# Performance work log

Measured on AMD Instinct MI355X. Metric: run time of the kernel, lower is better.

The kernel has to match this reference:

```python
import jax, jax.numpy as jnp
import numpy as np

N_NODES = 100000
N_EDGES = 1600000
D_IN = 128
D_OUT = 128


def setup_inputs() -> dict:
    key = jax.random.key(0)
    k1, k2, k3, k4, k5, k6 = jax.random.split(key, 6)
    x = jax.random.normal(k1, (N_NODES, D_IN), dtype=jnp.float32)
    edge_index = jax.random.randint(k2, (2, N_EDGES), 0, N_NODES, dtype=jnp.int64)
    edge_weight = jax.random.uniform(k3, (N_EDGES,), dtype=jnp.float32)
    # Linear(in_features=128, out_features=128, bias=True) parameters
    bound = 1.0 / np.sqrt(D_IN)
    W = jax.random.uniform(k4, (D_OUT, D_IN), minval=-bound, maxval=bound, dtype=jnp.float32)
    b = jax.random.uniform(k5, (D_OUT,), minval=-bound, maxval=bound, dtype=jnp.float32)
    return {
        "x": x,
        "edge_index": edge_index,
        "edge_weight": edge_weight,
        "W": W,
        "b": b,
        "vertex_cnt": N_NODES,
        "rule_cnt": 0,
    }


def reference(x, edge_index, edge_weight, W, b, vertex_cnt, rule_cnt):
    # KPropagate: edge-based message passing.
    # messages[e] = edge_weight[e] * x[src[e]]; out[dst] = sum of messages into dst.
    src = edge_index[0]
    dst = edge_index[1]
    msgs = x[src] * edge_weight[:, None]          # [E, D_IN]
    agg = jax.ops.segment_sum(msgs, dst, num_segments=vertex_cnt)  # [N, D_IN]
    # Dense linear projection: y = agg @ W^T + b
    return agg @ W.T + b
```

## Files before the change

kernel.cpp:

```cpp
#include <hip/hip_runtime.h>
#include <hip/hip_bf16.h>

#define D 128
#define RT 64
#define BK 64
#define CAP 2048
#define PAD 16

typedef __attribute__((ext_vector_type(8))) short short8;
typedef __attribute__((ext_vector_type(4))) float floatx4;

__device__ __forceinline__ ushort f2bf(float v) {
  return __hip_bfloat16_raw(__float2bfloat16(v)).x;
}
__device__ __forceinline__ float bf2f(ushort u) {
  return __uint_as_float((unsigned)u << 16);
}

__global__ __launch_bounds__(256) void k1_gemm_fill(
    const float* __restrict__ x, const float* __restrict__ W,
    ushort* __restrict__ y, const int* __restrict__ ei,
    const float* __restrict__ ew, int* __restrict__ cursor,
    int2* __restrict__ bucket, int N, int E, int GB) {
  if (blockIdx.x >= GB) {
    int e = (blockIdx.x - GB) * 256 + threadIdx.x;
    if (e < E) {
      int s = ei[e];
      int d = ei[E + e];
      float w = ew[e];
      int bk = d >> 6;
      int p = atomicAdd(&cursor[bk * PAD], 1);
      if (p < CAP)
        bucket[(long long)bk * CAP + p] =
            make_int2(s | ((d & 63) << 26), __float_as_int(w));
    }
    return;
  }
  __shared__ __align__(16) ushort sX[RT * 136];
  __shared__ __align__(16) ushort sW[128 * 136];

  int tid = threadIdx.x;
  int rowBase = blockIdx.x * RT;

#pragma unroll
  for (int it = 0; it < 16; it++) {
    int i = tid + it * 256;
    int r = i >> 5;
    int c4 = i & 31;
    float4 v = *(const float4*)(W + r * 128 + c4 * 4);
    *(ushort4*)&sW[r * 136 + c4 * 4] =
        make_ushort4(f2bf(v.x), f2bf(v.y), f2bf(v.z), f2bf(v.w));
  }
#pragma unroll
  for (int it = 0; it < 8; it++) {
    int i = tid + it * 256;
    int r = i >> 5;
    int c4 = i & 31;
    int row = rowBase + r;
    float4 v = (row < N) ? *(const float4*)(x + (long long)row * 128 + c4 * 4)
                         : make_float4(0.f, 0.f, 0.f, 0.f);
    *(ushort4*)&sX[r * 136 + c4 * 4] =
        make_ushort4(f2bf(v.x), f2bf(v.y), f2bf(v.z), f2bf(v.w));
  }
  __syncthreads();

  int wv = tid >> 6;
  int lane = tid & 63;
  int m = lane & 15;
  int q = lane >> 4;

  const ushort* aRow = &sX[(wv * 16 + m) * 136 + q * 8];
  const ushort* bRow = &sW[m * 136 + q * 8];

  floatx4 acc[8];
#pragma unroll
  for (int ct = 0; ct < 8; ct++) acc[ct] = (floatx4){0.f, 0.f, 0.f, 0.f};

#pragma unroll
  for (int ks = 0; ks < 4; ks++) {
    short8 a = *(const short8*)(aRow + ks * 32);
#pragma unroll
    for (int ct = 0; ct < 8; ct++) {
      short8 b = *(const short8*)(bRow + ct * 16 * 136 + ks * 32);
      acc[ct] = __builtin_amdgcn_mfma_f32_16x16x32_bf16(a, b, acc[ct], 0, 0, 0);
    }
  }

  int row0 = rowBase + wv * 16 + q * 4;
#pragma unroll
  for (int r = 0; r < 4; r++) {
    int row = row0 + r;
    if (row < N) {
      ushort* yp = y + (long long)row * 128 + m;
#pragma unroll
      for (int ct = 0; ct < 8; ct++) yp[ct * 16] = f2bf(acc[ct][r]);
    }
  }
}

__global__ __launch_bounds__(256) void sort_gather(
    const ushort* __restrict__ y, const int2* __restrict__ bucket,
    const int* __restrict__ cursor, const float* __restrict__ bias,
    float* __restrict__ out, int N) {
  __shared__ __align__(16) int2 smd[CAP];
  __shared__ int sdeg[BK];
  __shared__ int soffs[BK];
  __shared__ int scur[BK];

  int tid = threadIdx.x;
  int bk = blockIdx.x;
  long long base = (long long)bk * CAP;
  int cnt = min(cursor[bk * PAD], CAP);

  if (tid < BK) sdeg[tid] = 0;
  __syncthreads();
  for (int i = tid; i < cnt; i += 256) {
    unsigned v = (unsigned)bucket[base + i].x;
    atomicAdd(&sdeg[v >> 26], 1);
  }
  __syncthreads();
  if (tid < BK) {
    int s = 0;
    for (int j = 0; j < tid; j++) s += sdeg[j];
    soffs[tid] = s;
    scur[tid] = s;
  }
  __syncthreads();
  for (int i = tid; i < cnt; i += 256) {
    int2 md = bucket[base + i];
    int d = (unsigned)md.x >> 26;
    int pos = atomicAdd(&scur[d], 1);
    smd[pos] = md;
  }
  __syncthreads();

  int wv = tid >> 6;
  int lane = tid & 63;
  const ushort2* yv = (const ushort2*)y;
  float2 bb = ((const float2*)bias)[lane];

  for (int nd = wv; nd < BK; nd += 4) {
    int node = bk * BK + nd;
    if (node >= N) continue;
    int st = soffs[nd];
    int c = sdeg[nd];
    float ax = 0.f, ay = 0.f;
    int j = 0;
    for (; j + 4 <= c; j += 4) {
      int2 m0 = smd[st + j];
      int2 m1 = smd[st + j + 1];
      int2 m2 = smd[st + j + 2];
      int2 m3 = smd[st + j + 3];
      int s0 = m0.x & 0x03FFFFFF, s1 = m1.x & 0x03FFFFFF;
      int s2 = m2.x & 0x03FFFFFF, s3 = m3.x & 0x03FFFFFF;
      float w0 = __int_as_float(m0.y), w1 = __int_as_float(m1.y);
      float w2 = __int_as_float(m2.y), w3 = __int_as_float(m3.y);
      ushort2 u0 = yv[(long long)s0 * 64 + lane];
      ushort2 u1 = yv[(long long)s1 * 64 + lane];
      ushort2 u2 = yv[(long long)s2 * 64 + lane];
      ushort2 u3 = yv[(long long)s3 * 64 + lane];
      ax += w0 * bf2f(u0.x) + w1 * bf2f(u1.x) + w2 * bf2f(u2.x) +
            w3 * bf2f(u3.x);
      ay += w0 * bf2f(u0.y) + w1 * bf2f(u1.y) + w2 * bf2f(u2.y) +
            w3 * bf2f(u3.y);
    }
    for (; j < c; j++) {
      int2 m0 = smd[st + j];
      int s0 = m0.x & 0x03FFFFFF;
      float w0 = __int_as_float(m0.y);
      ushort2 u0 = yv[(long long)s0 * 64 + lane];
      ax += w0 * bf2f(u0.x);
      ay += w0 * bf2f(u0.y);
    }
    float2 o = {ax + bb.x, ay + bb.y};
    ((float2*)out)[(long long)node * 64 + lane] = o;
  }
}

extern "C" void kernel_launch(void* const* d_in, const int* in_sizes, int n_in,
                              void* d_out, int out_size, void* d_ws,
                              size_t ws_size, hipStream_t stream) {
  const float* x = (const float*)d_in[0];
  const int* ei = (const int*)d_in[1];
  const float* ew = (const float*)d_in[2];
  const float* W = (const float*)d_in[3];
  const float* b = (const float*)d_in[4];

  int N = in_sizes[0] / D;
  int E = in_sizes[2];
  int NBK = (N + BK - 1) / BK;

  int* cursor = (int*)d_ws;
  int2* bucket = (int2*)(cursor + (size_t)NBK * PAD);
  ushort* y = (ushort*)(bucket + (size_t)NBK * CAP);

  hipMemsetAsync(cursor, 0, (size_t)NBK * PAD * sizeof(int), stream);

  int GB = (N + RT - 1) / RT;
  int FB = (E + 255) / 256;
  k1_gemm_fill<<<GB + FB, 256, 0, stream>>>(x, W, y, ei, ew, cursor, bucket, N,
                                            E, GB);
  sort_gather<<<NBK, 256, 0, stream>>>(y, bucket, cursor, b, (float*)d_out, N);
}
```

Before: 301.7 us.

## Split bucket atomic cursors per XCD to avoid cross-die atomic contention

Each destination bucket now gets eight sub-buckets, one per XCD, selected by reading the hardware XCC_ID register. Edge-fill atomics then hit a cursor that only one die touches, which is meant to cut contended cross-die atomics and cache-line bouncing. The gather kernel walks all eight sub-buckets when building its shared-memory sort. Each sub-bucket holds at most 256 entries, so an uneven spread of edges across XCDs could overflow one and silently drop edges, and the cursor array grows eightfold.

```diff
diff --git a/kernel.cpp b/kernel.cpp
--- a/kernel.cpp
+++ b/kernel.cpp
@@ -5,6 +5,7 @@
 #define RT 64
 #define BK 64
 #define CAP 2048
+#define SUBCAP 256
 #define PAD 16
 
 typedef __attribute__((ext_vector_type(8))) short short8;
@@ -15,6 +16,12 @@
 }
 __device__ __forceinline__ float bf2f(ushort u) {
   return __uint_as_float((unsigned)u << 16);
+}
+
+__device__ __forceinline__ int xcd_id() {
+  int v;
+  asm volatile("s_getreg_b32 %0, hwreg(HW_REG_XCC_ID)" : "=s"(v));
+  return v & 7;
 }
 
 __global__ __launch_bounds__(256) void k1_gemm_fill(
@@ -23,15 +30,16 @@
     const float* __restrict__ ew, int* __restrict__ cursor,
     int2* __restrict__ bucket, int N, int E, int GB) {
   if (blockIdx.x >= GB) {
+    int sb = xcd_id();
     int e = (blockIdx.x - GB) * 256 + threadIdx.x;
     if (e < E) {
       int s = ei[e];
       int d = ei[E + e];
       float w = ew[e];
       int bk = d >> 6;
-      int p = atomicAdd(&cursor[bk * PAD], 1);
-      if (p < CAP)
-        bucket[(long long)bk * CAP + p] =
+      int p = atomicAdd(&cursor[(bk * 8 + sb) * PAD], 1);
+      if (p < SUBCAP)
+        bucket[(long long)bk * CAP + sb * SUBCAP + p] =
             make_int2(s | ((d & 63) << 26), __float_as_int(w));
     }
     return;
@@ -110,13 +118,16 @@
   int tid = threadIdx.x;
   int bk = blockIdx.x;
   long long base = (long long)bk * CAP;
-  int cnt = min(cursor[bk * PAD], CAP);
 
   if (tid < BK) sdeg[tid] = 0;
   __syncthreads();
-  for (int i = tid; i < cnt; i += 256) {
-    unsigned v = (unsigned)bucket[base + i].x;
-    atomicAdd(&sdeg[v >> 26], 1);
+#pragma unroll
+  for (int sb = 0; sb < 8; sb++) {
+    int c = min(cursor[(bk * 8 + sb) * PAD], SUBCAP);
+    for (int i = tid; i < c; i += 256) {
+      unsigned v = (unsigned)bucket[base + sb * SUBCAP + i].x;
+      atomicAdd(&sdeg[v >> 26], 1);
+    }
   }
   __syncthreads();
   if (tid < BK) {
@@ -126,11 +137,15 @@
     scur[tid] = s;
   }
   __syncthreads();
-  for (int i = tid; i < cnt; i += 256) {
-    int2 md = bucket[base + i];
-    int d = (unsigned)md.x >> 26;
-    int pos = atomicAdd(&scur[d], 1);
-    smd[pos] = md;
+#pragma unroll
+  for (int sb = 0; sb < 8; sb++) {
+    int c = min(cursor[(bk * 8 + sb) * PAD], SUBCAP);
+    for (int i = tid; i < c; i += 256) {
+      int2 md = bucket[base + sb * SUBCAP + i];
+      int d = (unsigned)md.x >> 26;
+      int pos = atomicAdd(&scur[d], 1);
+      smd[pos] = md;
+    }
   }
   __syncthreads();
 
@@ -191,10 +206,10 @@
   int NBK = (N + BK - 1) / BK;
 
   int* cursor = (int*)d_ws;
-  int2* bucket = (int2*)(cursor + (size_t)NBK * PAD);
+  int2* bucket = (int2*)(cursor + (size_t)NBK * 8 * PAD);
   ushort* y = (ushort*)(bucket + (size_t)NBK * CAP);
 
-  hipMemsetAsync(cursor, 0, (size_t)NBK * PAD * sizeof(int), stream);
+  hipMemsetAsync(cursor, 0, (size_t)NBK * 8 * PAD * sizeof(int), stream);
 
   int GB = (N + RT - 1) / RT;
   int FB = (E + 255) / 256;
```

After: 250.3 us. 17.0% less time.
